# Performance work log

Hardware: AMD Instinct MI355X
Metric: run time of the kernel (lower is better)

The kernel has to match this reference:

```python
import jax, jax.numpy as jnp
import numpy as np

HEADS = 8
IN_C = 256
MDL = 512
N = 4
L = 4096
NE = 65536  # avg degree 16


def setup_inputs() -> dict:
    key = jax.random.key(0)
    ks = jax.random.split(key, 14)
    f32 = jnp.float32
    s = 0.05
    return {
        "queries": jax.random.normal(ks[0], (N, L, IN_C), f32),
        "keys": jax.random.normal(ks[1], (N, L, IN_C), f32),
        "values": jax.random.normal(ks[2], (N, L, IN_C), f32),
        "adj": jax.random.randint(ks[3], (2, NE), 0, L, dtype=jnp.int32),
        "edge_pos_enc": jax.random.normal(ks[4], (N, HEADS, NE), f32),
        "Wq": jax.random.normal(ks[5], (IN_C, MDL), f32) * s,
        "bq": jnp.zeros((MDL,), f32),
        "Wk": jax.random.normal(ks[6], (IN_C, MDL), f32) * s,
        "bk": jnp.zeros((MDL,), f32),
        "Wv": jax.random.normal(ks[7], (IN_C, MDL), f32) * s,
        "bv": jnp.zeros((MDL,), f32),
        "Wo": jax.random.normal(ks[8], (MDL, MDL), f32) * s,
        "bo": jnp.zeros((MDL,), f32),
    }


def reference(queries, keys, values, adj, edge_pos_enc, Wq, bq, Wk, bk, Wv, bv, Wo, bo):
    n, l, _ = queries.shape
    h = HEADS
    e = MDL // h  # per-head dim
    temp = 1.0 / jnp.sqrt(jnp.asarray(e, queries.dtype))
    dst, src = adj[0], adj[1]

    def split(x):  # (n, l, mdl) -> (n*h, l, e)
        return x.reshape(n, l, h, e).transpose(0, 2, 1, 3).reshape(n * h, l, e)

    q = split(queries @ Wq + bq)
    k = split(keys @ Wk + bk)
    v = split(values @ Wv + bv)
    epe = edge_pos_enc.reshape(n * h, NE)

    def head(qh, kh, vh, eh):
        # qh,kh,vh: (l, e); eh: (Ne,)
        scores = temp * (jnp.sum(qh[dst] * kh[src], axis=-1) + eh)  # (Ne,)
        m = jax.ops.segment_max(scores, dst, num_segments=l)
        p = jnp.exp(scores - m[dst])
        z = jax.ops.segment_sum(p, dst, num_segments=l)
        alpha = p / z[dst]  # segment softmax keyed by dst (adj[0])
        return jax.ops.segment_sum(alpha[:, None] * vh[src], dst, num_segments=l)  # (l, e)

    out = jax.vmap(head)(q, k, v, epe)  # (n*h, l, e)
    out = out.reshape(n, h, l, e).transpose(0, 2, 1, 3).reshape(n, l, h * e)
    return out @ Wo + bo
```

## Files before the change

kernel.cpp:

```cpp
#include <hip/hip_runtime.h>
#include <hip/hip_bf16.h>
#include <math.h>
#include <stdint.h>

#define HEADS 8
#define IN_C  256
#define MDL   512
#define NB    4
#define LL    4096
#define NE    65536
#define EDIM  64
#define TEMP  0.125f

typedef __bf16 bf16x8 __attribute__((ext_vector_type(8)));
typedef float  f32x4  __attribute__((ext_vector_type(4)));
typedef short  short8 __attribute__((ext_vector_type(8)));

__device__ __forceinline__ void glds16(const void* g, void* l) {
    __builtin_amdgcn_global_load_lds(
        (const __attribute__((address_space(1))) void*)g,
        (__attribute__((address_space(3))) void*)l, 16, 0, 0);
}

__device__ __forceinline__ short8 cvt8(float4 a, float4 b) {
    union { short8 v; __hip_bfloat16 h[8]; } u;
    u.h[0] = __float2bfloat16(a.x); u.h[1] = __float2bfloat16(a.y);
    u.h[2] = __float2bfloat16(a.z); u.h[3] = __float2bfloat16(a.w);
    u.h[4] = __float2bfloat16(b.x); u.h[5] = __float2bfloat16(b.y);
    u.h[6] = __float2bfloat16(b.z); u.h[7] = __float2bfloat16(b.w);
    return u.v;
}

__global__ __launch_bounds__(256) void gemm_qkv(
    const float* __restrict__ A0, const float* __restrict__ A1,
    const float* __restrict__ A2,
    const __hip_bfloat16* __restrict__ B0, const __hip_bfloat16* __restrict__ B1,
    const __hip_bfloat16* __restrict__ B2,
    const float* __restrict__ b0, const float* __restrict__ b1,
    const float* __restrict__ b2,
    __hip_bfloat16* __restrict__ C0, __hip_bfloat16* __restrict__ C1,
    __hip_bfloat16* __restrict__ C2)
{
    __shared__ __align__(16) __hip_bfloat16 As[128 * 64];
    __shared__ __align__(16) __hip_bfloat16 Bs[128 * 64];

    const int K = IN_C, N = MDL;
    const int lin  = blockIdx.x;
    const int xcd  = lin & 7;
    const int t    = lin >> 3;
    const int z    = t >> 6;
    const int rest = t & 63;
    const int bm   = (xcd * 16 + (rest & 15)) * 128;
    const int bn   = (rest >> 4) * 128;

    const float* A           = (z == 0) ? A0 : (z == 1) ? A1 : A2;
    const __hip_bfloat16* Bt = (z == 0) ? B0 : (z == 1) ? B1 : B2;
    const float* bias        = (z == 0) ? b0 : (z == 1) ? b1 : b2;
    __hip_bfloat16* C        = (z == 0) ? C0 : (z == 1) ? C1 : C2;

    const int tid  = threadIdx.x;
    const int lane = tid & 63;
    const int w    = tid >> 6;
    const int wr   = w >> 1, wc = w & 1;

    const float*          gA[4];
    const __hip_bfloat16* gB[4];
    __hip_bfloat16* lAw[4];
    __hip_bfloat16* lB[4];
    #pragma unroll
    for (int it = 0; it < 4; it++) {
        int idx  = it * 256 + tid;
        int r    = idx >> 3;
        int cpos = idx & 7;
        int cdat = cpos ^ (r & 7);
        gA[it]  = A  + (size_t)(bm + r) * K + cdat * 8;
        gB[it]  = Bt + (size_t)(bn + r) * K + cdat * 8;
        lAw[it] = As + r * 64 + cpos * 8;
        lB[it]  = Bs + (size_t)(it * 256 + w * 64) * 8;
    }

    int fa[2][4], fb[2][4];
    #pragma unroll
    for (int kk = 0; kk < 2; kk++)
        #pragma unroll
        for (int i = 0; i < 4; i++) {
            int rA = wr * 64 + i * 16 + (lane & 15);
            int gc = kk * 4 + (lane >> 4);
            fa[kk][i] = rA * 64 + (gc ^ (rA & 7)) * 8;
            int rB = wc * 64 + i * 16 + (lane & 15);
            fb[kk][i] = rB * 64 + (gc ^ (rB & 7)) * 8;
        }

    f32x4 acc[4][4] = {};

    for (int k0 = 0; k0 < K; k0 += 64) {
        #pragma unroll
        for (int it = 0; it < 4; it++) glds16(gB[it] + k0, lB[it]);
        #pragma unroll
        for (int it = 0; it < 4; it++) {
            float4 a = *(const float4*)(gA[it] + k0);
            float4 b = *(const float4*)(gA[it] + k0 + 4);
            *(short8*)lAw[it] = cvt8(a, b);
        }
        __syncthreads();

        #pragma unroll
        for (int kk = 0; kk < 2; kk++) {
            bf16x8 av[4], bv[4];
            #pragma unroll
            for (int i = 0; i < 4; i++) av[i] = *(const bf16x8*)(As + fa[kk][i]);
            #pragma unroll
            for (int i = 0; i < 4; i++) bv[i] = *(const bf16x8*)(Bs + fb[kk][i]);
            #pragma unroll
            for (int mi = 0; mi < 4; mi++)
                #pragma unroll
                for (int ni = 0; ni < 4; ni++)
                    acc[mi][ni] = __builtin_amdgcn_mfma_f32_16x16x32_bf16(
                        av[mi], bv[ni], acc[mi][ni], 0, 0, 0);
        }
        __syncthreads();
    }

    #pragma unroll
    for (int mi = 0; mi < 4; mi++) {
        int row = bm + wr * 64 + mi * 16 + (lane >> 4) * 4;
        #pragma unroll
        for (int ni = 0; ni < 4; ni++) {
            int col = bn + wc * 64 + ni * 16 + (lane & 15);
            float bb = bias[col];
            #pragma unroll
            for (int j = 0; j < 4; j++)
                C[(size_t)(row + j) * N + col] = __float2bfloat16(acc[mi][ni][j] + bb);
        }
    }
}

__global__ __launch_bounds__(256) void gemm_out(
    const __hip_bfloat16* __restrict__ A, const __hip_bfloat16* __restrict__ Bt,
    const float* __restrict__ bias, float* __restrict__ C)
{
    __shared__ __align__(16) __hip_bfloat16 As[64 * 64];
    __shared__ __align__(16) __hip_bfloat16 Bs[128 * 64];

    const int K = MDL, N = MDL;
    const int lin = blockIdx.x;
    const int xcd = lin & 7;
    const int t   = lin >> 3;
    const int bm  = (xcd * 32 + (t & 31)) * 64;
    const int bn  = (t >> 5) * 128;

    const int tid  = threadIdx.x;
    const int lane = tid & 63;
    const int w    = tid >> 6;
    const int wr   = w >> 1, wc = w & 1;

    const __hip_bfloat16* gA[2];
    __hip_bfloat16* lA[2];
    #pragma unroll
    for (int it = 0; it < 2; it++) {
        int idx = it * 256 + tid;
        int r = idx >> 3;
        int c = (idx & 7) ^ (r & 7);
        gA[it] = A + (size_t)(bm + r) * K + c * 8;
        lA[it] = As + (size_t)(it * 256 + w * 64) * 8;
    }
    const __hip_bfloat16* gB[4];
    __hip_bfloat16* lB[4];
    #pragma unroll
    for (int it = 0; it < 4; it++) {
        int idx = it * 256 + tid;
        int r = idx >> 3;
        int c = (idx & 7) ^ (r & 7);
        gB[it] = Bt + (size_t)(bn + r) * K + c * 8;
        lB[it] = Bs + (size_t)(it * 256 + w * 64) * 8;
    }

    int fa[2][2], fb[2][4];
    #pragma unroll
    for (int kk = 0; kk < 2; kk++) {
        int gc = kk * 4 + (lane >> 4);
        #pragma unroll
        for (int i = 0; i < 2; i++) {
            int rA = wr * 32 + i * 16 + (lane & 15);
            fa[kk][i] = rA * 64 + (gc ^ (rA & 7)) * 8;
        }
        #pragma unroll
        for (int i = 0; i < 4; i++) {
            int rB = wc * 64 + i * 16 + (lane & 15);
            fb[kk][i] = rB * 64 + (gc ^ (rB & 7)) * 8;
        }
    }

    f32x4 acc[2][4] = {};

    for (int k0 = 0; k0 < K; k0 += 64) {
        #pragma unroll
        for (int it = 0; it < 2; it++) glds16(gA[it] + k0, lA[it]);
        #pragma unroll
        for (int it = 0; it < 4; it++) glds16(gB[it] + k0, lB[it]);
        __syncthreads();

        #pragma unroll
        for (int kk = 0; kk < 2; kk++) {
            bf16x8 av[2], bv[4];
            #pragma unroll
            for (int i = 0; i < 2; i++) av[i] = *(const bf16x8*)(As + fa[kk][i]);
            #pragma unroll
            for (int i = 0; i < 4; i++) bv[i] = *(const bf16x8*)(Bs + fb[kk][i]);
            #pragma unroll
            for (int mi = 0; mi < 2; mi++)
                #pragma unroll
                for (int ni = 0; ni < 4; ni++)
                    acc[mi][ni] = __builtin_amdgcn_mfma_f32_16x16x32_bf16(
                        av[mi], bv[ni], acc[mi][ni], 0, 0, 0);
        }
        __syncthreads();
    }

    #pragma unroll
    for (int mi = 0; mi < 2; mi++) {
        int row = bm + wr * 32 + mi * 16 + (lane >> 4) * 4;
        #pragma unroll
        for (int ni = 0; ni < 4; ni++) {
            int col = bn + wc * 64 + ni * 16 + (lane & 15);
            float bb = bias[col];
            #pragma unroll
            for (int j = 0; j < 4; j++)
                C[(size_t)(row + j) * N + col] = acc[mi][ni][j] + bb;
        }
    }
}

__global__ __launch_bounds__(1024) void csr_build(
    const int* __restrict__ dst, int* __restrict__ offsets,
    int* __restrict__ cursor, int* __restrict__ reorder)
{
    __shared__ int hist[4096];
    __shared__ int wsum[16];
    __shared__ int bcnt[9], boff[9];
    const int tid  = threadIdx.x;
    const int lane = tid & 63;
    const int wid  = tid >> 6;

    #pragma unroll
    for (int i = 0; i < 4; i++) hist[tid + i * 1024] = 0;
    if (tid < 9) bcnt[tid] = 0;
    __syncthreads();

    const int4* d4 = (const int4*)dst;
    #pragma unroll
    for (int i = 0; i < 16; i++) {
        int4 v = d4[i * 1024 + tid];
        atomicAdd(&hist[v.x], 1);
        atomicAdd(&hist[v.y], 1);
        atomicAdd(&hist[v.z], 1);
        atomicAdd(&hist[v.w], 1);
    }
    __syncthreads();

    int c[4];
    int base = tid * 4;
    int s = 0;
    #pragma unroll
    for (int i = 0; i < 4; i++) { c[i] = hist[base + i]; s += c[i]; }

    int v = s;
    #pragma unroll
    for (int off = 1; off < 64; off <<= 1) {
        int t = __shfl_up(v, off);
        if (lane >= off) v += t;
    }
    if (lane == 63) wsum[wid] = v;
    __syncthreads();
    if (wid == 0) {
        int wv = (lane < 16) ? wsum[lane] : 0;
        #pragma unroll
        for (int off = 1; off < 16; off <<= 1) {
            int t = __shfl_up(wv, off);
            if (lane >= off) wv += t;
        }
        if (lane < 16) wsum[lane] = wv;
    }
    __syncthreads();

    int prefix = (wid > 0 ? wsum[wid - 1] : 0) + (v - s);
    int run = prefix;
    int mybk[4];
    #pragma unroll
    for (int i = 0; i < 4; i++) {
        offsets[base + i] = run;
        cursor[base + i]  = run;
        run += c[i];
        int sc = (c[i] + 7) >> 3; if (sc > 8) sc = 8;
        mybk[i] = 8 - sc;
        atomicAdd(&bcnt[mybk[i]], 1);
    }
    if (tid == 1023) offsets[4096] = run;
    __syncthreads();
    if (tid == 0) {
        int acc0 = 0;
        #pragma unroll
        for (int b = 0; b < 9; b++) { boff[b] = acc0; acc0 += bcnt[b]; }
    }
    __syncthreads();
    #pragma unroll
    for (int i = 0; i < 4; i++) {
        int pos = atomicAdd(&boff[mybk[i]], 1);
        reorder[pos] = base + i;
    }
}

__global__ __launch_bounds__(256) void prep(
    const int* __restrict__ dst, const int* __restrict__ srcarr,
    const float* __restrict__ epe, int* __restrict__ cursor,
    int* __restrict__ src_s, float* __restrict__ epe_s,
    const float* __restrict__ Wq, const float* __restrict__ Wk,
    const float* __restrict__ Wv, const float* __restrict__ Wo,
    __hip_bfloat16* __restrict__ Wqt, __hip_bfloat16* __restrict__ Wkt,
    __hip_bfloat16* __restrict__ Wvt, __hip_bfloat16* __restrict__ Wot)
{
    __shared__ float t[32][33];
    const int b = blockIdx.x;

    if (b < 256) {
        int e = b * 256 + threadIdx.x;
        int p = atomicAdd(&cursor[dst[e]], 1);
        src_s[p] = srcarr[e];
        #pragma unroll
        for (int n = 0; n < NB; n++) {
            float4 a2, b2;
            const float* base = epe + (size_t)(n * HEADS) * NE + e;
            a2.x = base[0 * NE]; a2.y = base[1 * NE]; a2.z = base[2 * NE]; a2.w = base[3 * NE];
            b2.x = base[4 * NE]; b2.y = base[5 * NE]; b2.z = base[6 * NE]; b2.w = base[7 * NE];
            float* o = epe_s + ((size_t)n * NE + p) * 8;
            *(float4*)o       = a2;
            *(float4*)(o + 4) = b2;
        }
    } else {
        int bb = b - 256;
        const float* W; __hip_bfloat16* Wt; int K, tt;
        if (bb < 384) {
            int m = bb >> 7; tt = bb & 127; K = IN_C;
            W  = (m == 0) ? Wq  : (m == 1) ? Wk  : Wv;
            Wt = (m == 0) ? Wqt : (m == 1) ? Wkt : Wvt;
        } else {
            tt = bb - 384; K = MDL; W = Wo; Wt = Wot;
        }
        const int N = MDL;
        int bx = (tt & 15) * 32;
        int by = (tt >> 4) * 32;
        int tx = threadIdx.x & 31, ty = threadIdx.x >> 5;
        #pragma unroll
        for (int i = 0; i < 4; i++)
            t[ty + i * 8][tx] = W[(size_t)(by + ty + i * 8) * N + bx + tx];
        __syncthreads();
        #pragma unroll
        for (int i = 0; i < 4; i++)
            Wt[(size_t)(bx + ty + i * 8) * K + by + tx] =
                __float2bfloat16(t[tx][ty + i * 8]);
    }
}

__global__ __launch_bounds__(256) void sparse_score(
    const __hip_bfloat16* __restrict__ Qb, const __hip_bfloat16* __restrict__ Kb,
    const int* __restrict__ src_s, const float* __restrict__ epe_s,
    const int* __restrict__ offsets, const int* __restrict__ reorder,
    float* __restrict__ score_s, float2* __restrict__ mz)
{
    const int lane = threadIdx.x & 63;
    const int wid  = threadIdx.x >> 6;
    const int bid  = blockIdx.x;
    const int xcd  = bid & 7;
    const int n    = xcd >> 1;
    const int base = ((bid >> 3) << 1) | (xcd & 1);
    const int dstn = reorder[(base << 2) | wid];
    const int task = n * LL + dstn;
    const int hg   = lane >> 3;

    const int beg = offsets[dstn];
    const int end = offsets[dstn + 1];
    const int deg = end - beg;
    if (deg == 0) return;

    bf16x8 q8 = *(const bf16x8*)(Qb + (size_t)task * MDL + lane * 8);
    float qf[8];
    #pragma unroll
    for (int j = 0; j < 8; j++) qf[j] = (float)q8[j];

    const __hip_bfloat16* Kn = Kb + (size_t)n * LL * MDL + lane * 8;
    const float* pe_n = epe_s + (size_t)n * NE * 8 + hg;
    float* sc_n = score_s + (size_t)n * NE * 8 + hg;

    float m = -INFINITY, z = 0.0f;

    if (deg <= 64) {
        const int my_src = src_s[beg + ((lane < deg) ? lane : (deg - 1))];

        #pragma unroll
        for (int slot = 0; slot < 8; slot++) {
            const int r0 = slot * 8;
            if (r0 < deg) {
                bf16x8 kk[8];
                #pragma unroll
                for (int j = 0; j < 8; j++) {
                    int s = __shfl(my_src, r0 + j);
                    kk[j] = *(const bf16x8*)(Kn + (size_t)s * MDL);
                }
                const int rel_mine = r0 + (lane & 7);
                float pp = (rel_mine < deg)
                         ? pe_n[(size_t)(beg + rel_mine) * 8] : -INFINITY;

                float p[8];
                #pragma unroll
                for (int j = 0; j < 8; j++) {
                    float d = 0.0f;
                    #pragma unroll
                    for (int dd = 0; dd < 8; dd++)
                        d = fmaf(qf[dd], (float)kk[j][dd], d);
                    p[j] = d;
                }
                float n0, n1, n2, n3, u0, u1, sraw;
                {
                    float a0 = (lane & 1) ? p[1] : p[0];
                    float b0 = (lane & 1) ? p[0] : p[1];
                    n0 = a0 + __shfl_xor(b0, 1);
                    float a1 = (lane & 1) ? p[3] : p[2];
                    float b1 = (lane & 1) ? p[2] : p[3];
                    n1 = a1 + __shfl_xor(b1, 1);
                    float a2 = (lane & 1) ? p[5] : p[4];
                    float b2 = (lane & 1) ? p[4] : p[5];
                    n2 = a2 + __shfl_xor(b2, 1);
                    float a3 = (lane & 1) ? p[7] : p[6];
                    float b3 = (lane & 1) ? p[6] : p[7];
                    n3 = a3 + __shfl_xor(b3, 1);

                    float c0 = (lane & 2) ? n1 : n0;
                    float d0 = (lane & 2) ? n0 : n1;
                    u0 = c0 + __shfl_xor(d0, 2);
                    float c1 = (lane & 2) ? n3 : n2;
                    float d1 = (lane & 2) ? n2 : n3;
                    u1 = c1 + __shfl_xor(d1, 2);

                    float e0 = (lane & 4) ? u1 : u0;
                    float f0 = (lane & 4) ? u0 : u1;
                    sraw = e0 + __shfl_xor(f0, 4);
                }

                float sc_my = TEMP * (sraw + pp);
                if (rel_mine < deg)
                    sc_n[(size_t)(beg + rel_mine) * 8] = sc_my;

                float gm = sc_my;
                gm = fmaxf(gm, __shfl_xor(gm, 1));
                gm = fmaxf(gm, __shfl_xor(gm, 2));
                gm = fmaxf(gm, __shfl_xor(gm, 4));
                float mnew = fmaxf(m, gm);
                float e_my = __expf(sc_my - mnew);
                float gs = e_my;
                gs += __shfl_xor(gs, 1);
                gs += __shfl_xor(gs, 2);
                gs += __shfl_xor(gs, 4);
                z = z * __expf(m - mnew) + gs;
                m = mnew;
            }
        }
    } else {
        for (int i = beg; i < end; i += 4) {
            float sc4[4];
            #pragma unroll
            for (int j = 0; j < 4; j++) {
                int idx = i + j;
                int ok  = idx < end;
                int s   = ok ? src_s[idx] : src_s[beg];
                bf16x8 kk = *(const bf16x8*)(Kn + (size_t)s * MDL);
                float pp = ok ? pe_n[(size_t)idx * 8] : -INFINITY;
                float d = 0.0f;
                #pragma unroll
                for (int dd = 0; dd < 8; dd++) d += qf[dd] * (float)kk[dd];
                d += __shfl_xor(d, 1);
                d += __shfl_xor(d, 2);
                d += __shfl_xor(d, 4);
                sc4[j] = TEMP * (d + pp);
                if (ok && (lane & 7) == 0)
                    sc_n[(size_t)idx * 8] = sc4[j];
            }
            float mb   = fmaxf(fmaxf(sc4[0], sc4[1]), fmaxf(sc4[2], sc4[3]));
            float mnew = fmaxf(m, mb);
            float sc   = __expf(m - mnew);
            float s0 = __expf(sc4[0] - mnew);
            float s1 = __expf(sc4[1] - mnew);
            float s2 = __expf(sc4[2] - mnew);
            float s3 = __expf(sc4[3] - mnew);
            z = z * sc + (s0 + s1 + s2 + s3);
            m = mnew;
        }
    }

    if ((lane & 7) == 0) {
        float2 v; v.x = m; v.y = 1.0f / z;
        mz[(size_t)task * 8 + hg] = v;
    }
}

__global__ __launch_bounds__(256) void sparse_out(
    const __hip_bfloat16* __restrict__ Vb,
    const int* __restrict__ src_s, const float* __restrict__ score_s,
    const int* __restrict__ offsets, const int* __restrict__ reorder,
    const float2* __restrict__ mz, __hip_bfloat16* __restrict__ O)
{
    const int lane = threadIdx.x & 63;
    const int wid  = threadIdx.x >> 6;
    const int bid  = blockIdx.x;
    const int xcd  = bid & 7;
    const int n    = xcd >> 1;
    const int base = ((bid >> 3) << 1) | (xcd & 1);
    const int dstn = reorder[(base << 2) | wid];
    const int task = n * LL + dstn;
    const int hg   = lane >> 3;

    const size_t rowbase = (size_t)task * MDL;
    const int beg = offsets[dstn];
    const int end = offsets[dstn + 1];
    const int deg = end - beg;

    union { short8 v8; __hip_bfloat16 h[8]; } uo;
    if (deg == 0) {
        #pragma unroll
        for (int j = 0; j < 8; j++) uo.h[j] = __float2bfloat16(0.0f);
        *(short8*)(O + rowbase + lane * 8) = uo.v8;
        return;
    }

    float2 mzv = mz[(size_t)task * 8 + hg];
    const float m = mzv.x, zinv = mzv.y;

    const __hip_bfloat16* Vn = Vb + (size_t)n * LL * MDL + lane * 8;
    const float* sc_n = score_s + (size_t)n * NE * 8 + hg;

    float acc[8] = {};

    if (deg <= 64) {
        const int my_src = src_s[beg + ((lane < deg) ? lane : (deg - 1))];

        #pragma unroll
        for (int slot = 0; slot < 8; slot++) {
            const int r0 = slot * 8;
            if (r0 < deg) {
                bf16x8 vv[8];
                #pragma unroll
                for (int j = 0; j < 8; j++) {
                    int s = __shfl(my_src, r0 + j);
                    vv[j] = *(const bf16x8*)(Vn + (size_t)s * MDL);
                }
                const int rel_mine = r0 + (lane & 7);
                float sc = (rel_mine < deg)
                         ? sc_n[(size_t)(beg + rel_mine) * 8] : -INFINITY;
                float a_l = __expf(sc - m) * zinv;
                #pragma unroll
                for (int j = 0; j < 8; j++) {
                    float al = __shfl(a_l, (lane & 56) | j);
                    #pragma unroll
                    for (int dd = 0; dd < 8; dd++)
                        acc[dd] = fmaf(al, (float)vv[j][dd], acc[dd]);
                }
            }
        }
    } else {
        for (int i = beg; i < end; i += 4) {
            #pragma unroll
            for (int j = 0; j < 4; j++) {
                int idx = i + j;
                int ok  = idx < end;
                int s   = ok ? src_s[idx] : src_s[beg];
                bf16x8 vv = *(const bf16x8*)(Vn + (size_t)s * MDL);
                float sc = ok ? sc_n[(size_t)idx * 8] : -INFINITY;
                float al = __expf(sc - m) * zinv;
                #pragma unroll
                for (int dd = 0; dd < 8; dd++)
                    acc[dd] = fmaf(al, (float)vv[dd], acc[dd]);
            }
        }
    }

    #pragma unroll
    for (int j = 0; j < 8; j++) uo.h[j] = __float2bfloat16(acc[j]);
    *(short8*)(O + rowbase + lane * 8) = uo.v8;
}

extern "C" void kernel_launch(void* const* d_in, const int* in_sizes, int n_in,
                              void* d_out, int out_size, void* d_ws, size_t ws_size,
                              hipStream_t stream)
{
    const float* queries = (const float*)d_in[0];
    const float* keys    = (const float*)d_in[1];
    const float* values  = (const float*)d_in[2];
    const int*   adj     = (const int*)d_in[3];
    const float* epe     = (const float*)d_in[4];
    const float* Wq = (const float*)d_in[5];
    const float* bq = (const float*)d_in[6];
    const float* Wk = (const float*)d_in[7];
    const float* bk = (const float*)d_in[8];
    const float* Wv = (const float*)d_in[9];
    const float* bv = (const float*)d_in[10];
    const float* Wo = (const float*)d_in[11];
    const float* bo = (const float*)d_in[12];
    float* out = (float*)d_out;

    const int* dst = adj;
    const int* src = adj + NE;

    const int    M   = NB * LL;
    const size_t NLM = (size_t)M * MDL;

    char* w = (char*)d_ws;
    __hip_bfloat16* Qb  = (__hip_bfloat16*)w; w += NLM * 2;
    __hip_bfloat16* Kb  = (__hip_bfloat16*)w; w += NLM * 2;
    __hip_bfloat16* Vb  = (__hip_bfloat16*)w; w += NLM * 2;
    __hip_bfloat16* Ob  = (__hip_bfloat16*)w; w += NLM * 2;
    __hip_bfloat16* Wqt = (__hip_bfloat16*)w; w += (size_t)MDL * IN_C * 2;
    __hip_bfloat16* Wkt = (__hip_bfloat16*)w; w += (size_t)MDL * IN_C * 2;
    __hip_bfloat16* Wvt = (__hip_bfloat16*)w; w += (size_t)MDL * IN_C * 2;
    __hip_bfloat16* Wot = (__hip_bfloat16*)w; w += (size_t)MDL * MDL * 2;
    int* offsets = (int*)w; w += 4100 * sizeof(int);
    int* cursor  = (int*)w; w += 4096 * sizeof(int);
    int* reorder = (int*)w; w += 4096 * sizeof(int);
    int*   src_s = (int*)w; w += NE * sizeof(int);
    float* epe_s   = (float*)w;  w += (size_t)NB * NE * 8 * sizeof(float);
    float* score_s = (float*)w;  w += (size_t)NB * NE * 8 * sizeof(float);
    float2* mz     = (float2*)w; w += (size_t)M * 8 * sizeof(float2);

    csr_build<<<1, 1024, 0, stream>>>(dst, offsets, cursor, reorder);

    prep<<<896, 256, 0, stream>>>(dst, src, epe, cursor, src_s, epe_s,
                                  Wq, Wk, Wv, Wo, Wqt, Wkt, Wvt, Wot);

    gemm_qkv<<<1536, 256, 0, stream>>>(queries, keys, values, Wqt, Wkt, Wvt,
                                       bq, bk, bv, Qb, Kb, Vb);

    sparse_score<<<(NB * LL) / 4, 256, 0, stream>>>(Qb, Kb, src_s, epe_s,
                                                    offsets, reorder, score_s, mz);
    sparse_out<<<(NB * LL) / 4, 256, 0, stream>>>(Vb, src_s, score_s,
                                                  offsets, reorder, mz, Ob);

    gemm_out<<<1024, 256, 0, stream>>>(Ob, Wot, bo, out);
}
```

Measured before the change: 116.6 us.

## Stage full-K weight panels in LDS and stream A fragments directly from global

Both projection GEMMs now load the entire K extent of the weight tile into shared memory once, behind a single barrier. A operand fragments are read straight from global memory into registers, with fp32-to-bf16 conversion in registers for the QKV GEMM, so the A tile is no longer staged in LDS. This removes the per-K-step barriers and the A shared-memory round trip. The output GEMM tile shape changes to 128x64 with each wave owning 32 rows. The cost is much larger LDS use per block (64KB), which may reduce occupancy, plus uncoalesced per-lane global reads for A with no software prefetch.

```diff
diff --git a/kernel.cpp b/kernel.cpp
--- a/kernel.cpp
+++ b/kernel.cpp
@@ -22,8 +22,8 @@
         (__attribute__((address_space(3))) void*)l, 16, 0, 0);
 }
 
-__device__ __forceinline__ short8 cvt8(float4 a, float4 b) {
-    union { short8 v; __hip_bfloat16 h[8]; } u;
+__device__ __forceinline__ bf16x8 cvt8b(float4 a, float4 b) {
+    union { short8 s; bf16x8 v; __hip_bfloat16 h[8]; } u;
     u.h[0] = __float2bfloat16(a.x); u.h[1] = __float2bfloat16(a.y);
     u.h[2] = __float2bfloat16(a.z); u.h[3] = __float2bfloat16(a.w);
     u.h[4] = __float2bfloat16(b.x); u.h[5] = __float2bfloat16(b.y);
@@ -41,8 +41,7 @@
     __hip_bfloat16* __restrict__ C0, __hip_bfloat16* __restrict__ C1,
     __hip_bfloat16* __restrict__ C2)
 {
-    __shared__ __align__(16) __hip_bfloat16 As[128 * 64];
-    __shared__ __align__(16) __hip_bfloat16 Bs[128 * 64];
+    __shared__ __align__(16) __hip_bfloat16 Bs[128 * 256];
 
     const int K = IN_C, N = MDL;
     const int lin  = blockIdx.x;
@@ -63,62 +62,51 @@
     const int w    = tid >> 6;
     const int wr   = w >> 1, wc = w & 1;
 
-    const float*          gA[4];
-    const __hip_bfloat16* gB[4];
-    __hip_bfloat16* lAw[4];
-    __hip_bfloat16* lB[4];
-    #pragma unroll
-    for (int it = 0; it < 4; it++) {
-        int idx  = it * 256 + tid;
-        int r    = idx >> 3;
-        int cpos = idx & 7;
-        int cdat = cpos ^ (r & 7);
-        gA[it]  = A  + (size_t)(bm + r) * K + cdat * 8;
-        gB[it]  = Bt + (size_t)(bn + r) * K + cdat * 8;
-        lAw[it] = As + r * 64 + cpos * 8;
-        lB[it]  = Bs + (size_t)(it * 256 + w * 64) * 8;
-    }
-
-    int fa[2][4], fb[2][4];
-    #pragma unroll
-    for (int kk = 0; kk < 2; kk++)
-        #pragma unroll
-        for (int i = 0; i < 4; i++) {
-            int rA = wr * 64 + i * 16 + (lane & 15);
-            int gc = kk * 4 + (lane >> 4);
-            fa[kk][i] = rA * 64 + (gc ^ (rA & 7)) * 8;
-            int rB = wc * 64 + i * 16 + (lane & 15);
-            fb[kk][i] = rB * 64 + (gc ^ (rB & 7)) * 8;
-        }
+    #pragma unroll
+    for (int i = 0; i < 16; i++) {
+        int idx  = i * 256 + tid;
+        int rr   = idx >> 5;
+        int cpos = idx & 31;
+        int cdat = cpos ^ (rr & 7);
+        glds16(Bt + (size_t)(bn + rr) * K + cdat * 8, Bs + rr * 256 + cpos * 8);
+    }
+
+    const float* ap[4];
+    #pragma unroll
+    for (int mi = 0; mi < 4; mi++) {
+        int rowA = bm + wr * 64 + mi * 16 + (lane & 15);
+        ap[mi] = A + (size_t)rowA * K + (lane >> 4) * 8;
+    }
+    int rB[4];
+    #pragma unroll
+    for (int ni = 0; ni < 4; ni++) rB[ni] = wc * 64 + ni * 16 + (lane & 15);
+
+    __syncthreads();
 
     f32x4 acc[4][4] = {};
 
-    for (int k0 = 0; k0 < K; k0 += 64) {
-        #pragma unroll
-        for (int it = 0; it < 4; it++) glds16(gB[it] + k0, lB[it]);
-        #pragma unroll
-        for (int it = 0; it < 4; it++) {
-            float4 a = *(const float4*)(gA[it] + k0);
-            float4 b = *(const float4*)(gA[it] + k0 + 4);
-            *(short8*)lAw[it] = cvt8(a, b);
-        }
-        __syncthreads();
-
-        #pragma unroll
-        for (int kk = 0; kk < 2; kk++) {
-            bf16x8 av[4], bv[4];
+    #pragma unroll
+    for (int kc = 0; kc < 8; kc++) {
+        bf16x8 am[4];
+        #pragma unroll
+        for (int mi = 0; mi < 4; mi++) {
+            float4 x = *(const float4*)(ap[mi] + kc * 32);
+            float4 y = *(const float4*)(ap[mi] + kc * 32 + 4);
+            am[mi] = cvt8b(x, y);
+        }
+        bf16x8 bv[4];
+        const int cbase = kc * 4 + (lane >> 4);
+        #pragma unroll
+        for (int ni = 0; ni < 4; ni++) {
+            int pos = cbase ^ (rB[ni] & 7);
+            bv[ni] = *(const bf16x8*)(Bs + rB[ni] * 256 + pos * 8);
+        }
+        #pragma unroll
+        for (int mi = 0; mi < 4; mi++)
             #pragma unroll
-            for (int i = 0; i < 4; i++) av[i] = *(const bf16x8*)(As + fa[kk][i]);
-            #pragma unroll
-            for (int i = 0; i < 4; i++) bv[i] = *(const bf16x8*)(Bs + fb[kk][i]);
-            #pragma unroll
-            for (int mi = 0; mi < 4; mi++)
-                #pragma unroll
-                for (int ni = 0; ni < 4; ni++)
-                    acc[mi][ni] = __builtin_amdgcn_mfma_f32_16x16x32_bf16(
-                        av[mi], bv[ni], acc[mi][ni], 0, 0, 0);
-        }
-        __syncthreads();
+            for (int ni = 0; ni < 4; ni++)
+                acc[mi][ni] = __builtin_amdgcn_mfma_f32_16x16x32_bf16(
+                    am[mi], bv[ni], acc[mi][ni], 0, 0, 0);
     }
 
     #pragma unroll
@@ -139,90 +127,69 @@
     const __hip_bfloat16* __restrict__ A, const __hip_bfloat16* __restrict__ Bt,
     const float* __restrict__ bias, float* __restrict__ C)
 {
-    __shared__ __align__(16) __hip_bfloat16 As[64 * 64];
-    __shared__ __align__(16) __hip_bfloat16 Bs[128 * 64];
+    __shared__ __align__(16) __hip_bfloat16 Bs[64 * 512];
 
     const int K = MDL, N = MDL;
     const int lin = blockIdx.x;
     const int xcd = lin & 7;
     const int t   = lin >> 3;
-    const int bm  = (xcd * 32 + (t & 31)) * 64;
-    const int bn  = (t >> 5) * 128;
+    const int bm  = (xcd * 16 + (t & 15)) * 128;
+    const int bn  = (t >> 4) * 64;
 
     const int tid  = threadIdx.x;
     const int lane = tid & 63;
     const int w    = tid >> 6;
-    const int wr   = w >> 1, wc = w & 1;
-
-    const __hip_bfloat16* gA[2];
-    __hip_bfloat16* lA[2];
-    #pragma unroll
-    for (int it = 0; it < 2; it++) {
-        int idx = it * 256 + tid;
-        int r = idx >> 3;
-        int c = (idx & 7) ^ (r & 7);
-        gA[it] = A + (size_t)(bm + r) * K + c * 8;
-        lA[it] = As + (size_t)(it * 256 + w * 64) * 8;
-    }
-    const __hip_bfloat16* gB[4];
-    __hip_bfloat16* lB[4];
-    #pragma unroll
-    for (int it = 0; it < 4; it++) {
-        int idx = it * 256 + tid;
-        int r = idx >> 3;
-        int c = (idx & 7) ^ (r & 7);
-        gB[it] = Bt + (size_t)(bn + r) * K + c * 8;
-        lB[it] = Bs + (size_t)(it * 256 + w * 64) * 8;
-    }
-
-    int fa[2][2], fb[2][4];
-    #pragma unroll
-    for (int kk = 0; kk < 2; kk++) {
-        int gc = kk * 4 + (lane >> 4);
-        #pragma unroll
-        for (int i = 0; i < 2; i++) {
-            int rA = wr * 32 + i * 16 + (lane & 15);
-            fa[kk][i] = rA * 64 + (gc ^ (rA & 7)) * 8;
-        }
-        #pragma unroll
-        for (int i = 0; i < 4; i++) {
-            int rB = wc * 64 + i * 16 + (lane & 15);
-            fb[kk][i] = rB * 64 + (gc ^ (rB & 7)) * 8;
-        }
-    }
+
+    #pragma unroll
+    for (int i = 0; i < 16; i++) {
+        int idx  = i * 256 + tid;
+        int rr   = idx >> 6;
+        int cpos = idx & 63;
+        int cdat = cpos ^ (rr & 7);
+        glds16(Bt + (size_t)(bn + rr) * K + cdat * 8, Bs + rr * 512 + cpos * 8);
+    }
+
+    const __hip_bfloat16* ap[2];
+    #pragma unroll
+    for (int mi = 0; mi < 2; mi++) {
+        int rowA = bm + w * 32 + mi * 16 + (lane & 15);
+        ap[mi] = A + (size_t)rowA * K + (lane >> 4) * 8;
+    }
+    int rB[4];
+    #pragma unroll
+    for (int ni = 0; ni < 4; ni++) rB[ni] = ni * 16 + (lane & 15);
+
+    __syncthreads();
 
     f32x4 acc[2][4] = {};
 
-    for (int k0 = 0; k0 < K; k0 += 64) {
-        #pragma unroll
-        for (int it = 0; it < 2; it++) glds16(gA[it] + k0, lA[it]);
-        #pragma unroll
-        for (int it = 0; it < 4; it++) glds16(gB[it] + k0, lB[it]);
-        __syncthreads();
-
-        #pragma unroll
-        for (int kk = 0; kk < 2; kk++) {
-            bf16x8 av[2], bv[4];
+    #pragma unroll
+    for (int kc = 0; kc < 16; kc++) {
+        bf16x8 am[2];
+        #pragma unroll
+        for (int mi = 0; mi < 2; mi++)
+            am[mi] = *(const bf16x8*)(ap[mi] + kc * 32);
+        bf16x8 bv[4];
+        const int cbase = kc * 4 + (lane >> 4);
+        #pragma unroll
+        for (int ni = 0; ni < 4; ni++) {
+            int pos = cbase ^ (rB[ni] & 7);
+            bv[ni] = *(const bf16x8*)(Bs + rB[ni] * 512 + pos * 8);
+        }
+        #pragma unroll
+        for (int mi = 0; mi < 2; mi++)
             #pragma unroll
-            for (int i = 0; i < 2; i++) av[i] = *(const bf16x8*)(As + fa[kk][i]);
-            #pragma unroll
-            for (int i = 0; i < 4; i++) bv[i] = *(const bf16x8*)(Bs + fb[kk][i]);
-            #pragma unroll
-            for (int mi = 0; mi < 2; mi++)
-                #pragma unroll
-                for (int ni = 0; ni < 4; ni++)
-                    acc[mi][ni] = __builtin_amdgcn_mfma_f32_16x16x32_bf16(
-                        av[mi], bv[ni], acc[mi][ni], 0, 0, 0);
-        }
-        __syncthreads();
+            for (int ni = 0; ni < 4; ni++)
+                acc[mi][ni] = __builtin_amdgcn_mfma_f32_16x16x32_bf16(
+                    am[mi], bv[ni], acc[mi][ni], 0, 0, 0);
     }
 
     #pragma unroll
     for (int mi = 0; mi < 2; mi++) {
-        int row = bm + wr * 32 + mi * 16 + (lane >> 4) * 4;
+        int row = bm + w * 32 + mi * 16 + (lane >> 4) * 4;
         #pragma unroll
         for (int ni = 0; ni < 4; ni++) {
-            int col = bn + wc * 64 + ni * 16 + (lane & 15);
+            int col = bn + ni * 16 + (lane & 15);
             float bb = bias[col];
             #pragma unroll
             for (int j = 0; j < 4; j++)
```

After: 148.1 us. +27.0%, slower.
